# Kernel optimization log

Hardware: AMD Instinct MI355X
Metric: run time of the kernel (lower is better)

Reference implementation:

```python
import jax, jax.numpy as jnp
import numpy as np

D = 768
H = 12
HD = 64
S = 77
FF = 3072
EPS = 1e-5


def _layernorm(x, w, b):
    mu = jnp.mean(x, axis=-1, keepdims=True)
    var = jnp.mean(jnp.square(x - mu), axis=-1, keepdims=True)
    return (x - mu) * jax.lax.rsqrt(var + EPS) * w + b


def setup_inputs() -> dict:
    key = jax.random.key(0)
    ks = jax.random.split(key, 18)
    s = 1.0 / np.sqrt(D)
    sf = 1.0 / np.sqrt(FF)
    return {
        "x": jax.random.normal(ks[0], (512, S, D), dtype=jnp.float32),
        "ln1_w": jnp.ones((D,), jnp.float32),
        "ln1_b": jnp.zeros((D,), jnp.float32),
        "qw": jax.random.uniform(ks[1], (D, D), jnp.float32, -s, s),
        "qb": jax.random.uniform(ks[2], (D,), jnp.float32, -s, s),
        "kw": jax.random.uniform(ks[3], (D, D), jnp.float32, -s, s),
        "kb": jax.random.uniform(ks[4], (D,), jnp.float32, -s, s),
        "vw": jax.random.uniform(ks[5], (D, D), jnp.float32, -s, s),
        "vb": jax.random.uniform(ks[6], (D,), jnp.float32, -s, s),
        "ow": jax.random.uniform(ks[7], (D, D), jnp.float32, -s, s),
        "ob": jax.random.uniform(ks[8], (D,), jnp.float32, -s, s),
        "ln2_w": jnp.ones((D,), jnp.float32),
        "ln2_b": jnp.zeros((D,), jnp.float32),
        "fc1_w": jax.random.uniform(ks[9], (FF, D), jnp.float32, -s, s),
        "fc1_b": jax.random.uniform(ks[10], (FF,), jnp.float32, -s, s),
        "fc2_w": jax.random.uniform(ks[11], (D, FF), jnp.float32, -sf, sf),
        "fc2_b": jax.random.uniform(ks[12], (D,), jnp.float32, -sf, sf),
    }


def reference(x, ln1_w, ln1_b, qw, qb, kw, kb, vw, vb, ow, ob,
              ln2_w, ln2_b, fc1_w, fc1_b, fc2_w, fc2_b):
    B = x.shape[0]
    # --- attention block ---
    h = _layernorm(x, ln1_w, ln1_b)
    q = (h @ qw.T + qb) * 0.125
    k = h @ kw.T + kb
    v = h @ vw.T + vb
    # [B, S, H, HD] -> [B, H, S, HD]
    q = q.reshape(B, S, H, HD).transpose(0, 2, 1, 3)
    k = k.reshape(B, S, H, HD).transpose(0, 2, 1, 3)
    v = v.reshape(B, S, H, HD).transpose(0, 2, 1, 3)
    scores = jnp.einsum('bhqd,bhkd->bhqk', q, k)  # [B,H,S,S]
    # causal additive mask: -inf strictly above diagonal
    mask = jnp.triu(jnp.full((S, S), -jnp.inf, dtype=scores.dtype), 1)
    scores = scores + mask
    attn = jax.nn.softmax(scores, axis=-1)
    ctx = jnp.einsum('bhqk,bhkd->bhqd', attn, v)  # [B,H,S,HD]
    ctx = ctx.transpose(0, 2, 1, 3).reshape(B, S, D)
    x = x + (ctx @ ow.T + ob)
    # --- MLP block with QuickGELU ---
    res = x
    h2 = _layernorm(x, ln2_w, ln2_b) @ fc1_w.T + fc1_b
    h2 = h2 * jax.nn.sigmoid(h2 * 1.702)
    return res + (h2 @ fc2_w.T + fc2_b)
```

## Files before the change

kernel.cpp:

```cpp
#include <hip/hip_runtime.h>

typedef unsigned short u16;
typedef __bf16 v8bf __attribute__((ext_vector_type(8)));
typedef unsigned short u16x8 __attribute__((ext_vector_type(8)));
typedef float v4f __attribute__((ext_vector_type(4)));

#define DEV __device__ __forceinline__

constexpr int M_TOK = 512 * 77;

DEV u16 f2bf(float f) {
  union { float f; unsigned int u; } v; v.f = f;
  unsigned int r = v.u + 0x7fffu + ((v.u >> 16) & 1u);
  return (u16)(r >> 16);
}

DEV void gload16(const void* g, void* l) {
  __builtin_amdgcn_global_load_lds((const __attribute__((address_space(1))) void*)g,
                                   (__attribute__((address_space(3))) void*)l, 16, 0, 0);
}

DEV v4f MF(v8bf a, v8bf b, v4f c) {
  return __builtin_amdgcn_mfma_f32_16x16x32_bf16(a, b, c, 0, 0, 0);
}

__global__ void cvt4_k(const float* __restrict__ src, u16* __restrict__ dst, int n4, float scale) {
  int i = blockIdx.x * blockDim.x + threadIdx.x;
  if (i >= n4) return;
  const float4 v = ((const float4*)src)[i];
  ushort4 o;
  o.x = f2bf(v.x * scale); o.y = f2bf(v.y * scale);
  o.z = f2bf(v.z * scale); o.w = f2bf(v.w * scale);
  ((ushort4*)dst)[i] = o;
}

__global__ void qkvb_k(const float* __restrict__ qb, const float* __restrict__ kb,
                       const float* __restrict__ vb, float* __restrict__ dst) {
  int i = blockIdx.x * 256 + threadIdx.x;
  if (i >= 2304) return;
  dst[i] = (i < 768) ? qb[i] * 0.125f : (i < 1536 ? kb[i - 768] : vb[i - 1536]);
}

__global__ __launch_bounds__(256) void ln_k(const float* __restrict__ x, const float* __restrict__ w,
                                            const float* __restrict__ bvec, u16* __restrict__ out, int nrows) {
  const int lane = threadIdx.x & 63;
  const int row = blockIdx.x * 4 + (threadIdx.x >> 6);
  if (row >= nrows) return;
  const float4* xr = (const float4*)(x + (size_t)row * 768);
  float4 v[3];
  float sum = 0.f, sq = 0.f;
#pragma unroll
  for (int t = 0; t < 3; ++t) {
    v[t] = xr[lane + 64 * t];
    sum += v[t].x + v[t].y + v[t].z + v[t].w;
    sq  += v[t].x * v[t].x + v[t].y * v[t].y + v[t].z * v[t].z + v[t].w * v[t].w;
  }
#pragma unroll
  for (int o = 1; o < 64; o <<= 1) { sum += __shfl_xor(sum, o, 64); sq += __shfl_xor(sq, o, 64); }
  const float mean = sum * (1.f / 768.f);
  const float inv = rsqrtf(sq * (1.f / 768.f) - mean * mean + 1e-5f);
  u16* orow = out + (size_t)row * 768;
#pragma unroll
  for (int t = 0; t < 3; ++t) {
    const int c = 4 * (lane + 64 * t);
    ushort4 o4;
    o4.x = f2bf((v[t].x - mean) * inv * w[c + 0] + bvec[c + 0]);
    o4.y = f2bf((v[t].y - mean) * inv * w[c + 1] + bvec[c + 1]);
    o4.z = f2bf((v[t].z - mean) * inv * w[c + 2] + bvec[c + 2]);
    o4.w = f2bf((v[t].w - mean) * inv * w[c + 3] + bvec[c + 3]);
    *(ushort4*)(orow + c) = o4;
  }
}

template <int OUTF32, int ACT, int RES>
__global__ __launch_bounds__(256, 2) void gemm128_k(
    const u16* __restrict__ A, const u16* __restrict__ Bw,
    const float* __restrict__ bias, const float* __restrict__ res,
    void* __restrict__ out, int M, int N, int K, int nbx) {
  __shared__ u16 lds[32768];
  const int tid = threadIdx.x;
  const int lane = tid & 63;
  const int wv = tid >> 6;
  const int wr = wv >> 1, wc = wv & 1;

  const int nwg = gridDim.x;
  const int q8 = nwg >> 3, r8 = nwg & 7;
  const int xcd = blockIdx.x & 7, cidx = blockIdx.x >> 3;
  const int wg = (xcd < r8 ? xcd * (q8 + 1) : r8 * (q8 + 1) + (xcd - r8) * q8) + cidx;
  const int m0 = (wg / nbx) * 128;
  const int n0 = (wg % nbx) * 128;

  const int frow = lane & 15, fq = lane >> 4;
  const int e = frow & 7;
  const int aB0 = (wr * 64 + frow) * 64 + ((fq ^ e) * 8);
  const int bB0 = 8192 + (wc * 64 + frow) * 64 + ((fq ^ e) * 8);

  const int srow = tid >> 3;
  const int cOff = ((tid & 7) ^ (srow & 7)) * 8;
  const u16* pA = A + (size_t)(m0 + srow) * K + cOff;
  const u16* pB = Bw + (size_t)(n0 + srow) * K + cOff;
  const size_t K32 = (size_t)K * 32;
  const int ldsW = wv * 512;

#define LD(IDX) (*(const v8bf*)&lds[IDX])
#define BAR() asm volatile("s_barrier" ::: "memory")
#define VM8() asm volatile("s_waitcnt vmcnt(8)" ::: "memory")
#define VM0() asm volatile("s_waitcnt vmcnt(0)" ::: "memory")
#define STA(kt) do { const int sb_ = ((kt) & 1) << 14;                              \
    gload16(pA + 0 * K32 + (size_t)(kt) * 64, &lds[sb_ + 0 * 2048 + ldsW]);         \
    gload16(pA + 1 * K32 + (size_t)(kt) * 64, &lds[sb_ + 1 * 2048 + ldsW]);         \
    gload16(pA + 2 * K32 + (size_t)(kt) * 64, &lds[sb_ + 2 * 2048 + ldsW]);         \
    gload16(pA + 3 * K32 + (size_t)(kt) * 64, &lds[sb_ + 3 * 2048 + ldsW]); } while (0)
#define STB(kt) do { const int sb_ = (((kt) & 1) << 14) + 8192;                     \
    gload16(pB + 0 * K32 + (size_t)(kt) * 64, &lds[sb_ + 0 * 2048 + ldsW]);         \
    gload16(pB + 1 * K32 + (size_t)(kt) * 64, &lds[sb_ + 1 * 2048 + ldsW]);         \
    gload16(pB + 2 * K32 + (size_t)(kt) * 64, &lds[sb_ + 2 * 2048 + ldsW]);         \
    gload16(pB + 3 * K32 + (size_t)(kt) * 64, &lds[sb_ + 3 * 2048 + ldsW]); } while (0)

  v4f acc[4][4];
#pragma unroll
  for (int i = 0; i < 4; ++i)
#pragma unroll
    for (int j = 0; j < 4; ++j) acc[i][j] = (v4f){0.f, 0.f, 0.f, 0.f};

  const int NT = K >> 6;

  STA(0); STB(0);
  STA(1); STB(1);
  VM8(); BAR();

#define ITER(kt, STG, VM)                                                       \
  do {                                                                          \
    const int sb = ((kt) & 1) << 14;                                            \
    v8bf a0 = LD(sb + aB0), a1 = LD(sb + aB0 + 1024);                           \
    v8bf a2 = LD(sb + aB0 + 2048), a3 = LD(sb + aB0 + 3072);                    \
    v8bf a4 = LD(sb + (aB0 ^ 32)), a5 = LD(sb + (aB0 ^ 32) + 1024);             \
    v8bf a6 = LD(sb + (aB0 ^ 32) + 2048), a7 = LD(sb + (aB0 ^ 32) + 3072);      \
    v8bf b0 = LD(sb + bB0), b1 = LD(sb + bB0 + 1024);                           \
    v8bf b2 = LD(sb + bB0 + 2048), b3 = LD(sb + bB0 + 3072);                    \
    v8bf b4 = LD(sb + (bB0 ^ 32)), b5 = LD(sb + (bB0 ^ 32) + 1024);             \
    v8bf b6 = LD(sb + (bB0 ^ 32) + 2048), b7 = LD(sb + (bB0 ^ 32) + 3072);      \
    asm volatile("s_waitcnt lgkmcnt(0)" ::: "memory");                          \
    BAR();             \
    if (STG) { STA((kt) + 2); STB((kt) + 2); }                                  \
    if ((VM) == 8) VM8(); else if ((VM) == 0) VM0();                            \
    __builtin_amdgcn_s_setprio(1);                                              \
    acc[0][0] = MF(a0, b0, acc[0][0]); acc[0][1] = MF(a0, b1, acc[0][1]);       \
    acc[0][2] = MF(a0, b2, acc[0][2]); acc[0][3] = MF(a0, b3, acc[0][3]);       \
    acc[1][0] = MF(a1, b0, acc[1][0]); acc[1][1] = MF(a1, b1, acc[1][1]);       \
    acc[1][2] = MF(a1, b2, acc[1][2]); acc[1][3] = MF(a1, b3, acc[1][3]);       \
    acc[2][0] = MF(a2, b0, acc[2][0]); acc[2][1] = MF(a2, b1, acc[2][1]);       \
    acc[2][2] = MF(a2, b2, acc[2][2]); acc[2][3] = MF(a2, b3, acc[2][3]);       \
    acc[3][0] = MF(a3, b0, acc[3][0]); acc[3][1] = MF(a3, b1, acc[3][1]);       \
    acc[3][2] = MF(a3, b2, acc[3][2]); acc[3][3] = MF(a3, b3, acc[3][3]);       \
    acc[0][0] = MF(a4, b4, acc[0][0]); acc[0][1] = MF(a4, b5, acc[0][1]);       \
    acc[0][2] = MF(a4, b6, acc[0][2]); acc[0][3] = MF(a4, b7, acc[0][3]);       \
    acc[1][0] = MF(a5, b4, acc[1][0]); acc[1][1] = MF(a5, b5, acc[1][1]);       \
    acc[1][2] = MF(a5, b6, acc[1][2]); acc[1][3] = MF(a5, b7, acc[1][3]);       \
    acc[2][0] = MF(a6, b4, acc[2][0]); acc[2][1] = MF(a6, b5, acc[2][1]);       \
    acc[2][2] = MF(a6, b6, acc[2][2]); acc[2][3] = MF(a6, b7, acc[2][3]);       \
    acc[3][0] = MF(a7, b4, acc[3][0]); acc[3][1] = MF(a7, b5, acc[3][1]);       \
    acc[3][2] = MF(a7, b6, acc[3][2]); acc[3][3] = MF(a7, b7, acc[3][3]);       \
    __builtin_amdgcn_s_setprio(0);                                              \
    BAR();              \
  } while (0)

  for (int kt = 0; kt < NT - 2; ++kt) ITER(kt, 1, 8);
  ITER(NT - 2, 0, 0);
  ITER(NT - 1, 0, -1);
#undef ITER
#undef LD
#undef BAR
#undef VM8
#undef VM0
#undef STA
#undef STB

#pragma unroll
  for (int i = 0; i < 4; ++i) {
    const int rowb = m0 + wr * 64 + i * 16 + fq * 4;
#pragma unroll
    for (int j = 0; j < 4; ++j) {
      const int col = n0 + wc * 64 + j * 16 + frow;
      const float bv = bias[col];
#pragma unroll
      for (int rr = 0; rr < 4; ++rr) {
        float v = acc[i][j][rr] + bv;
        if (ACT) v = v * (1.f / (1.f + __expf(-1.702f * v)));
        const size_t off = (size_t)(rowb + rr) * N + col;
        if (RES) v += res[off];
        if (OUTF32) ((float*)out)[off] = v;
        else ((u16*)out)[off] = f2bf(v);
      }
    }
  }
}

__global__ __launch_bounds__(256) void attn_k(const u16* __restrict__ qkv, u16* __restrict__ ctx) {
  __shared__ u16 sQK[10240];
  __shared__ u16 sVt[64 * 120];
  __shared__ float sS[80][81];
  const int tid = threadIdx.x;
  const int lane = tid & 63;
  const int wv = tid >> 6;
  const int b = blockIdx.x / 12;
  const int h = blockIdx.x % 12;
  u16* sQ = sQK;
  u16* sK = sQK + 5120;
  u16* sP = sQK;

  for (int i = tid; i < 10240 + 64 * 120; i += 256) {
    if (i < 10240) sQK[i] = 0; else sVt[i - 10240] = 0;
  }
  __syncthreads();

  const size_t tokBase = (size_t)(b * 77) * 2304 + h * 64;
  for (int c = tid; c < 77 * 8; c += 256) {
    const int row = c >> 3, k8 = (c & 7) * 8;
    const size_t src = tokBase + (size_t)row * 2304 + k8;
    *(u16x8*)&sQ[row * 64 + k8] = *(const u16x8*)&qkv[src];
    *(u16x8*)&sK[row * 64 + k8] = *(const u16x8*)&qkv[src + 768];
    u16x8 v = *(const u16x8*)&qkv[src + 1536];
#pragma unroll
    for (int j = 0; j < 8; ++j) sVt[(k8 + j) * 120 + row] = v[j];
  }
  __syncthreads();

  const int frow = lane & 15, fk = (lane >> 4) * 8;
  for (int t = wv; t < 25; t += 4) {
    const int it = t / 5, jt = t % 5;
    v4f acc = {0.f, 0.f, 0.f, 0.f};
#pragma unroll
    for (int kk = 0; kk < 2; ++kk) {
      v8bf a = *(const v8bf*)&sQ[(it * 16 + frow) * 64 + kk * 32 + fk];
      v8bf bb = *(const v8bf*)&sK[(jt * 16 + frow) * 64 + kk * 32 + fk];
      acc = MF(a, bb, acc);
    }
    const int col = jt * 16 + frow;
#pragma unroll
    for (int r = 0; r < 4; ++r) {
      const int row = it * 16 + (lane >> 4) * 4 + r;
      sS[row][col] = (col > row) ? -1e30f : acc[r];
    }
  }
  __syncthreads();

  if (tid < 80) {
    const int row = tid;
    float mx = -1e30f;
    for (int c2 = 0; c2 < 80; ++c2) mx = fmaxf(mx, sS[row][c2]);
    float sum = 0.f;
    for (int c2 = 0; c2 < 80; ++c2) { float e = __expf(sS[row][c2] - mx); sum += e; sS[row][c2] = e; }
    const float inv = 1.f / sum;
    for (int c2 = 0; c2 < 80; ++c2) sP[row * 96 + c2] = f2bf(sS[row][c2] * inv);
    for (int c2 = 80; c2 < 96; ++c2) sP[row * 96 + c2] = 0;
  }
  __syncthreads();

  const size_t outBase = (size_t)(b * 77) * 768 + h * 64;
  for (int t = wv; t < 20; t += 4) {
    const int it = t / 4, jt = t % 4;
    v4f acc = {0.f, 0.f, 0.f, 0.f};
#pragma unroll
    for (int kk = 0; kk < 3; ++kk) {
      v8bf a = *(const v8bf*)&sP[(it * 16 + frow) * 96 + kk * 32 + fk];
      v8bf bb = *(const v8bf*)&sVt[(jt * 16 + frow) * 120 + kk * 32 + fk];
      acc = MF(a, bb, acc);
    }
    const int col = jt * 16 + frow;
#pragma unroll
    for (int r = 0; r < 4; ++r) {
      const int row = it * 16 + (lane >> 4) * 4 + r;
      if (row < 77) ctx[outBase + (size_t)row * 768 + col] = f2bf(acc[r]);
    }
  }
}

extern "C" void kernel_launch(void* const* d_in, const int* in_sizes, int n_in,
                              void* d_out, int out_size, void* d_ws, size_t ws_size,
                              hipStream_t stream) {
  const float* x    = (const float*)d_in[0];
  const float* ln1w = (const float*)d_in[1];
  const float* ln1b = (const float*)d_in[2];
  const float* qw   = (const float*)d_in[3];
  const float* qb   = (const float*)d_in[4];
  const float* kw   = (const float*)d_in[5];
  const float* kb   = (const float*)d_in[6];
  const float* vw   = (const float*)d_in[7];
  const float* vb   = (const float*)d_in[8];
  const float* ow   = (const float*)d_in[9];
  const float* ob   = (const float*)d_in[10];
  const float* ln2w = (const float*)d_in[11];
  const float* ln2b = (const float*)d_in[12];
  const float* f1wf = (const float*)d_in[13];
  const float* f1b  = (const float*)d_in[14];
  const float* f2wf = (const float*)d_in[15];
  const float* f2b  = (const float*)d_in[16];
  float* outp = (float*)d_out;

  char* p = (char*)d_ws;
  auto alloc = [&](size_t bytes) { char* r = p; p += (bytes + 255) & ~(size_t)255; return r; };
  u16* wqkv = (u16*)alloc((size_t)2304 * 768 * 2);
  u16* owb  = (u16*)alloc((size_t)768 * 768 * 2);
  u16* f1w  = (u16*)alloc((size_t)3072 * 768 * 2);
  u16* f2w  = (u16*)alloc((size_t)768 * 3072 * 2);
  float* qkvb = (float*)alloc(2304 * 4);
  u16* bufA = (u16*)alloc((size_t)M_TOK * 768 * 2);
  u16* bufB = (u16*)alloc((size_t)M_TOK * 3072 * 2);

  cvt4_k<<<576, 256, 0, stream>>>(qw, wqkv, 147456, 0.125f);
  cvt4_k<<<576, 256, 0, stream>>>(kw, wqkv + 589824, 147456, 1.f);
  cvt4_k<<<576, 256, 0, stream>>>(vw, wqkv + 1179648, 147456, 1.f);
  cvt4_k<<<576, 256, 0, stream>>>(ow, owb, 147456, 1.f);
  cvt4_k<<<2304, 256, 0, stream>>>(f1wf, f1w, 589824, 1.f);
  cvt4_k<<<2304, 256, 0, stream>>>(f2wf, f2w, 589824, 1.f);
  qkvb_k<<<9, 256, 0, stream>>>(qb, kb, vb, qkvb);

  ln_k<<<M_TOK / 4, 256, 0, stream>>>(x, ln1w, ln1b, bufA, M_TOK);
  gemm128_k<0, 0, 0><<<308 * 18, 256, 0, stream>>>(bufA, wqkv, qkvb, nullptr, bufB, M_TOK, 2304, 768, 18);
  attn_k<<<512 * 12, 256, 0, stream>>>(bufB, bufA);
  gemm128_k<1, 0, 1><<<308 * 6, 256, 0, stream>>>(bufA, owb, ob, x, outp, M_TOK, 768, 768, 6);
  ln_k<<<M_TOK / 4, 256, 0, stream>>>(outp, ln2w, ln2b, bufA, M_TOK);
  gemm128_k<0, 1, 0><<<308 * 24, 256, 0, stream>>>(bufA, f1w, f1b, nullptr, bufB, M_TOK, 3072, 768, 24);
  gemm128_k<1, 0, 1><<<308 * 6, 256, 0, stream>>>(bufB, f2w, f2b, outp, outp, M_TOK, 768, 3072, 6);
}
```

Baseline: 940.7 us.

## Halve GEMM K-tile to 32 to cut LDS and raise occupancy to 4 blocks

The 128x128 bf16 GEMM now stages K-tiles of 32 instead of 64, halving shared memory from 64KB to 32KB and raising the launch bound from 2 to 4 blocks per CU. The LDS swizzle, load mapping and wait counts are adjusted for the narrower tile. Each barrier pair now covers only 16 MFMAs instead of 32, so synchronisation overhead per unit of compute doubles. The tighter launch bound may also force register pressure or spills.

```diff
diff --git a/kernel.cpp b/kernel.cpp
--- a/kernel.cpp
+++ b/kernel.cpp
@@ -73,11 +73,11 @@
 }
 
 template <int OUTF32, int ACT, int RES>
-__global__ __launch_bounds__(256, 2) void gemm128_k(
+__global__ __launch_bounds__(256, 4) void gemm128_k(
     const u16* __restrict__ A, const u16* __restrict__ Bw,
     const float* __restrict__ bias, const float* __restrict__ res,
     void* __restrict__ out, int M, int N, int K, int nbx) {
-  __shared__ u16 lds[32768];
+  __shared__ u16 lds[16384];
   const int tid = threadIdx.x;
   const int lane = tid & 63;
   const int wv = tid >> 6;
@@ -91,31 +91,27 @@
   const int n0 = (wg % nbx) * 128;
 
   const int frow = lane & 15, fq = lane >> 4;
-  const int e = frow & 7;
-  const int aB0 = (wr * 64 + frow) * 64 + ((fq ^ e) * 8);
-  const int bB0 = 8192 + (wc * 64 + frow) * 64 + ((fq ^ e) * 8);
-
-  const int srow = tid >> 3;
-  const int cOff = ((tid & 7) ^ (srow & 7)) * 8;
+  const int g8 = (fq ^ ((frow >> 1) & 3)) * 8;
+  const int aB = (wr * 64 + frow) * 32 + g8;
+  const int bB = 4096 + (wc * 64 + frow) * 32 + g8;
+
+  const int srow = tid >> 2;
+  const int cOff = ((tid & 3) ^ ((srow >> 1) & 3)) * 8;
   const u16* pA = A + (size_t)(m0 + srow) * K + cOff;
   const u16* pB = Bw + (size_t)(n0 + srow) * K + cOff;
-  const size_t K32 = (size_t)K * 32;
+  const size_t K64 = (size_t)K * 64;
   const int ldsW = wv * 512;
 
 #define LD(IDX) (*(const v8bf*)&lds[IDX])
 #define BAR() asm volatile("s_barrier" ::: "memory")
-#define VM8() asm volatile("s_waitcnt vmcnt(8)" ::: "memory")
+#define VM4() asm volatile("s_waitcnt vmcnt(4)" ::: "memory")
 #define VM0() asm volatile("s_waitcnt vmcnt(0)" ::: "memory")
-#define STA(kt) do { const int sb_ = ((kt) & 1) << 14;                              \
-    gload16(pA + 0 * K32 + (size_t)(kt) * 64, &lds[sb_ + 0 * 2048 + ldsW]);         \
-    gload16(pA + 1 * K32 + (size_t)(kt) * 64, &lds[sb_ + 1 * 2048 + ldsW]);         \
-    gload16(pA + 2 * K32 + (size_t)(kt) * 64, &lds[sb_ + 2 * 2048 + ldsW]);         \
-    gload16(pA + 3 * K32 + (size_t)(kt) * 64, &lds[sb_ + 3 * 2048 + ldsW]); } while (0)
-#define STB(kt) do { const int sb_ = (((kt) & 1) << 14) + 8192;                     \
-    gload16(pB + 0 * K32 + (size_t)(kt) * 64, &lds[sb_ + 0 * 2048 + ldsW]);         \
-    gload16(pB + 1 * K32 + (size_t)(kt) * 64, &lds[sb_ + 1 * 2048 + ldsW]);         \
-    gload16(pB + 2 * K32 + (size_t)(kt) * 64, &lds[sb_ + 2 * 2048 + ldsW]);         \
-    gload16(pB + 3 * K32 + (size_t)(kt) * 64, &lds[sb_ + 3 * 2048 + ldsW]); } while (0)
+#define STAGE(t, s) do { const int sb_ = (s) << 13;                                   \
+    gload16(pA + 0 * K64 + (size_t)(t) * 32, &lds[sb_ + 0 * 2048 + ldsW]);            \
+    gload16(pA + 1 * K64 + (size_t)(t) * 32, &lds[sb_ + 1 * 2048 + ldsW]);            \
+    gload16(pB + 0 * K64 + (size_t)(t) * 32, &lds[sb_ + 4096 + 0 * 2048 + ldsW]);     \
+    gload16(pB + 1 * K64 + (size_t)(t) * 32, &lds[sb_ + 4096 + 1 * 2048 + ldsW]);     \
+  } while (0)
 
   v4f acc[4][4];
 #pragma unroll
@@ -123,27 +119,22 @@
 #pragma unroll
     for (int j = 0; j < 4; ++j) acc[i][j] = (v4f){0.f, 0.f, 0.f, 0.f};
 
-  const int NT = K >> 6;
-
-  STA(0); STB(0);
-  STA(1); STB(1);
-  VM8(); BAR();
+  const int NT = K >> 5;
+
+  STAGE(0, 0); STAGE(1, 1);
+  VM4(); BAR();
 
 #define ITER(kt, STG, VM)                                                       \
   do {                                                                          \
-    const int sb = ((kt) & 1) << 14;                                            \
-    v8bf a0 = LD(sb + aB0), a1 = LD(sb + aB0 + 1024);                           \
-    v8bf a2 = LD(sb + aB0 + 2048), a3 = LD(sb + aB0 + 3072);                    \
-    v8bf a4 = LD(sb + (aB0 ^ 32)), a5 = LD(sb + (aB0 ^ 32) + 1024);             \
-    v8bf a6 = LD(sb + (aB0 ^ 32) + 2048), a7 = LD(sb + (aB0 ^ 32) + 3072);      \
-    v8bf b0 = LD(sb + bB0), b1 = LD(sb + bB0 + 1024);                           \
-    v8bf b2 = LD(sb + bB0 + 2048), b3 = LD(sb + bB0 + 3072);                    \
-    v8bf b4 = LD(sb + (bB0 ^ 32)), b5 = LD(sb + (bB0 ^ 32) + 1024);             \
-    v8bf b6 = LD(sb + (bB0 ^ 32) + 2048), b7 = LD(sb + (bB0 ^ 32) + 3072);      \
+    const int sb = ((kt) & 1) << 13;                                            \
+    v8bf a0 = LD(sb + aB),        a1 = LD(sb + aB + 512);                       \
+    v8bf a2 = LD(sb + aB + 1024), a3 = LD(sb + aB + 1536);                      \
+    v8bf b0 = LD(sb + bB),        b1 = LD(sb + bB + 512);                       \
+    v8bf b2 = LD(sb + bB + 1024), b3 = LD(sb + bB + 1536);                      \
     asm volatile("s_waitcnt lgkmcnt(0)" ::: "memory");                          \
     BAR();             \
-    if (STG) { STA((kt) + 2); STB((kt) + 2); }                                  \
-    if ((VM) == 8) VM8(); else if ((VM) == 0) VM0();                            \
+    if (STG) STAGE((kt) + 2, (kt) & 1);                                         \
+    if ((VM) == 4) VM4(); else if ((VM) == 0) VM0();                            \
     __builtin_amdgcn_s_setprio(1);                                              \
     acc[0][0] = MF(a0, b0, acc[0][0]); acc[0][1] = MF(a0, b1, acc[0][1]);       \
     acc[0][2] = MF(a0, b2, acc[0][2]); acc[0][3] = MF(a0, b3, acc[0][3]);       \
@@ -153,28 +144,19 @@
     acc[2][2] = MF(a2, b2, acc[2][2]); acc[2][3] = MF(a2, b3, acc[2][3]);       \
     acc[3][0] = MF(a3, b0, acc[3][0]); acc[3][1] = MF(a3, b1, acc[3][1]);       \
     acc[3][2] = MF(a3, b2, acc[3][2]); acc[3][3] = MF(a3, b3, acc[3][3]);       \
-    acc[0][0] = MF(a4, b4, acc[0][0]); acc[0][1] = MF(a4, b5, acc[0][1]);       \
-    acc[0][2] = MF(a4, b6, acc[0][2]); acc[0][3] = MF(a4, b7, acc[0][3]);       \
-    acc[1][0] = MF(a5, b4, acc[1][0]); acc[1][1] = MF(a5, b5, acc[1][1]);       \
-    acc[1][2] = MF(a5, b6, acc[1][2]); acc[1][3] = MF(a5, b7, acc[1][3]);       \
-    acc[2][0] = MF(a6, b4, acc[2][0]); acc[2][1] = MF(a6, b5, acc[2][1]);       \
-    acc[2][2] = MF(a6, b6, acc[2][2]); acc[2][3] = MF(a6, b7, acc[2][3]);       \
-    acc[3][0] = MF(a7, b4, acc[3][0]); acc[3][1] = MF(a7, b5, acc[3][1]);       \
-    acc[3][2] = MF(a7, b6, acc[3][2]); acc[3][3] = MF(a7, b7, acc[3][3]);       \
     __builtin_amdgcn_s_setprio(0);                                              \
     BAR();              \
   } while (0)
 
-  for (int kt = 0; kt < NT - 2; ++kt) ITER(kt, 1, 8);
+  for (int kt = 0; kt < NT - 2; ++kt) ITER(kt, 1, 4);
   ITER(NT - 2, 0, 0);
   ITER(NT - 1, 0, -1);
 #undef ITER
 #undef LD
 #undef BAR
-#undef VM8
+#undef VM4
 #undef VM0
-#undef STA
-#undef STB
+#undef STAGE
 
 #pragma unroll
   for (int i = 0; i < 4; ++i) {
@@ -250,7 +232,7 @@
     float mx = -1e30f;
     for (int c2 = 0; c2 < 80; ++c2) mx = fmaxf(mx, sS[row][c2]);
     float sum = 0.f;
-    for (int c2 = 0; c2 < 80; ++c2) { float e = __expf(sS[row][c2] - mx); sum += e; sS[row][c2] = e; }
+    for (int c2 = 0; c2 < 80; ++c2) { float e2 = __expf(sS[row][c2] - mx); sum += e2; sS[row][c2] = e2; }
     const float inv = 1.f / sum;
     for (int c2 = 0; c2 < 80; ++c2) sP[row * 96 + c2] = f2bf(sS[row][c2] * inv);
     for (int c2 = 80; c2 < 96; ++c2) sP[row * 96 + c2] = 0;
```

New measurement: 1.041 ms. +10.7%, slower.
